# Kernel tuning notes

Hardware: AMD Instinct MI355X
Metric: run time of the kernel (lower is better)

Reference implementation:

```python
import jax, jax.numpy as jnp
import numpy as np

EPS = 1e-5          # denominator epsilon from module
PROJ_EPS = 4e-3     # geoopt float32 projection epsilon
MIN_NORM = 1e-15


def _sabs(x):
    return jnp.abs(x) + MIN_NORM


def _sign(x):
    # geoopt sign: sign(0) == 1
    return jnp.sign(jnp.sign(x) + 0.5)


def _clamp_abs(x, eps):
    return _sign(x) * jnp.maximum(jnp.abs(x), eps)


def _lambda_x(x, k):
    # conformal factor 2 / (1 + k ||x||^2)
    return 2.0 / jnp.maximum(1.0 + k * jnp.sum(x * x, axis=-1, keepdims=True), MIN_NORM)


def _parallel_transport0back(x, v, k):
    # transport v at x back to the origin: v / (1 + k ||x||^2)
    return v / jnp.maximum(1.0 + k * jnp.sum(x * x, axis=-1, keepdims=True), MIN_NORM)


def _artan_k(x, k):
    sk = jnp.sqrt(_sabs(k))
    hyp = jnp.arctanh(jnp.minimum(sk * x, 1.0 - 1e-7)) / sk   # k < 0
    sph = jnp.arctan(sk * x) / sk                              # k > 0
    return jnp.where(k < 0, hyp, sph)


def _tan_k(x, k):
    sk = jnp.sqrt(_sabs(k))
    return jnp.where(k < 0, jnp.tanh(sk * x) / sk, jnp.tan(sk * x) / sk)


def _project(x, k):
    maxnorm = (1.0 - PROJ_EPS) / jnp.sqrt(_sabs(k))
    maxnorm = jnp.where(k < 0, maxnorm, 1e15)
    norm = jnp.maximum(jnp.linalg.norm(x, axis=-1, keepdims=True), MIN_NORM)
    return jnp.where(norm > maxnorm, x / norm * maxnorm, x)


def _mobius_scalar_mul(r, x, k):
    xn = jnp.maximum(jnp.linalg.norm(x, axis=-1, keepdims=True), MIN_NORM)
    return _tan_k(r * _artan_k(xn, k), k) * (x / xn)


def setup_inputs() -> dict:
    key = jax.random.key(0)
    kQ, kK, kV = jax.random.split(key, 3)
    B, H, N, D = 4, 16, 4096, 64
    Q = jax.random.normal(kQ, (B, H, N, D), dtype=jnp.float32)
    K = jax.random.normal(kK, (B, H, N, D), dtype=jnp.float32)
    # V holds points on the Poincare ball: scale so ||V|| < 1
    V = 0.05 * jax.random.normal(kV, (B, H, N, D), dtype=jnp.float32)
    mask = jnp.ones((N,), dtype=jnp.float32)
    c = jnp.array([-1.0], dtype=jnp.float32)  # hyperbolic curvature (geoopt k-convention)
    return {"Q": Q, "K": K, "V": V, "mask": mask, "c": c}


def reference(Q, K, V, mask, c):
    H = Q.shape[-3]
    curv = jnp.broadcast_to(c.reshape(-1), (H,)) if c.shape[0] == 1 else c
    curv = curv[:, None, None]  # [H,1,1] broadcasts over [B,H,N,D]

    x = V
    v1 = _parallel_transport0back(x, Q, curv)
    v2 = _parallel_transport0back(x, K, curv)
    gamma = _lambda_x(x, curv)                     # [B,H,N,1]
    denom = _clamp_abs(gamma - 1.0, 1e-10)
    m = mask[None, :, None]                        # [1,N,1]
    x = gamma / denom * x * m
    v1 = jax.nn.elu(v1) + 1.0
    v2 = denom * (jax.nn.elu(v2) + 1.0) * m

    v2_sum = jnp.sum(v2, axis=-2)                  # [B,H,D]
    D = jnp.einsum('...nd,...d->...n', v1, v2_sum)
    D_inv = 1.0 / jnp.where(D == 0, EPS, D)
    context = jnp.einsum('...nd,...ne->...de', v2, x)   # [B,H,D,D]
    X = jnp.einsum('...de,...nd,...n->...ne', context, v1, D_inv)

    X = _project(X, curv)
    X = _mobius_scalar_mul(0.5, X, curv)
    X = _project(X, curv)
    return X
```

## Files before the change

kernel.cpp:

```cpp
#include <hip/hip_runtime.h>
#include <math.h>

#define EPS_C      1e-05f
#define PROJ_EPS_C 0.004f
#define MIN_NORM_C 1e-15f

#define NTOK   4096
#define DH     64
#define TILE   64
#define CHUNK2 128
#define NCHUNK2 (NTOK / CHUNK2)
#define PADROW 68
#define SUB    16

#define FMA4(ACC, S, B)                      \
    ACC.x = fmaf((S), (B).x, ACC.x);         \
    ACC.y = fmaf((S), (B).y, ACC.y);         \
    ACC.z = fmaf((S), (B).z, ACC.z);         \
    ACC.w = fmaf((S), (B).w, ACC.w);

#define ADD4(ACC, B)                         \
    ACC.x += (B).x; ACC.y += (B).y;          \
    ACC.z += (B).z; ACC.w += (B).w;

__device__ __forceinline__ float elup(float z) {
    return z > 0.f ? z + 1.f : __expf(z);
}

__global__ __launch_bounds__(256, 4) void glin_phase1(
    const float* __restrict__ Kk, const float* __restrict__ Vv,
    const float* __restrict__ mask, const float* __restrict__ cc,
    int csize, int H, int chunk_toks, int BH,
    float* __restrict__ pt_out,
    float* __restrict__ part_v2, float* __restrict__ part_ctx)
{
    __shared__ __align__(16) float stg[4][2][SUB][PADROW];
    __shared__ __align__(16) float v2red[4][DH];

    const int bh    = blockIdx.x;
    const int chunk = blockIdx.y;
    const int h     = bh % H;
    const float k   = cc[(csize == 1) ? 0 : h];

    const float* Kp = Kk + (size_t)bh * NTOK * DH;
    const float* Vp = Vv + (size_t)bh * NTOK * DH;
    float* ptp      = pt_out + (size_t)bh * NTOK;

    const int tid  = threadIdx.x;
    const int w    = tid >> 6;
    const int lane = tid & 63;
    const int r    = lane >> 3;
    const int cg   = lane & 7;
    const int srow = lane >> 4;
    const int c4   = lane & 15;

    float (*v2w)[PADROW] = stg[w][0];
    float (*xsw)[PADROW] = stg[w][1];

    float4 acc[8][2];
#pragma unroll
    for (int i = 0; i < 8; ++i) {
        acc[i][0] = make_float4(0.f, 0.f, 0.f, 0.f);
        acc[i][1] = make_float4(0.f, 0.f, 0.f, 0.f);
    }
    float4 va0 = make_float4(0.f, 0.f, 0.f, 0.f);
    float4 va1 = make_float4(0.f, 0.f, 0.f, 0.f);

    const int wtok  = chunk_toks >> 2;
    const int wbase = chunk * chunk_toks + w * wtok;

    for (int s = 0; s < wtok; s += SUB) {
        asm volatile("s_waitcnt lgkmcnt(0)" ::: "memory");
        __builtin_amdgcn_sched_barrier(0);
#pragma unroll
        for (int p = 0; p < 4; ++p) {
            const int row  = p * 4 + srow;
            const int gtok = wbase + s + row;
            float4 v4 = *(const float4*)(Vp + (size_t)gtok * DH + c4 * 4);
            float4 k4 = *(const float4*)(Kp + (size_t)gtok * DH + c4 * 4);
            float ss = v4.x * v4.x + v4.y * v4.y + v4.z * v4.z + v4.w * v4.w;
            ss += __shfl_xor(ss, 1);
            ss += __shfl_xor(ss, 2);
            ss += __shfl_xor(ss, 4);
            ss += __shfl_xor(ss, 8);
            float dpt   = fmaxf(1.f + k * ss, MIN_NORM_C);
            float pt    = 1.f / dpt;
            float gamma = 2.f * pt;
            float gm1   = gamma - 1.f;
            float sg    = (gm1 < 0.f) ? -1.f : 1.f;
            float denomG = sg * fmaxf(fabsf(gm1), 1e-10f);
            float m     = mask[gtok];
            float xsc   = gamma / denomG * m;
            float a2    = denomG * m;
            if (c4 == 0) ptp[gtok] = pt;
            v4.x *= xsc; v4.y *= xsc; v4.z *= xsc; v4.w *= xsc;
            k4.x = a2 * elup(k4.x * pt);
            k4.y = a2 * elup(k4.y * pt);
            k4.z = a2 * elup(k4.z * pt);
            k4.w = a2 * elup(k4.w * pt);
            *(float4*)&xsw[row][c4 * 4] = v4;
            *(float4*)&v2w[row][c4 * 4] = k4;
        }
        asm volatile("s_waitcnt lgkmcnt(0)" ::: "memory");
        __builtin_amdgcn_sched_barrier(0);
#pragma unroll 4
        for (int t = 0; t < SUB; ++t) {
            const float4 a0 = *(const float4*)&v2w[t][r * 8];
            const float4 a1 = *(const float4*)&v2w[t][r * 8 + 4];
            const float4 b0 = *(const float4*)&xsw[t][cg * 8];
            const float4 b1 = *(const float4*)&xsw[t][cg * 8 + 4];
            ADD4(va0, a0);
            ADD4(va1, a1);
            FMA4(acc[0][0], a0.x, b0); FMA4(acc[0][1], a0.x, b1);
            FMA4(acc[1][0], a0.y, b0); FMA4(acc[1][1], a0.y, b1);
            FMA4(acc[2][0], a0.z, b0); FMA4(acc[2][1], a0.z, b1);
            FMA4(acc[3][0], a0.w, b0); FMA4(acc[3][1], a0.w, b1);
            FMA4(acc[4][0], a1.x, b0); FMA4(acc[4][1], a1.x, b1);
            FMA4(acc[5][0], a1.y, b0); FMA4(acc[5][1], a1.y, b1);
            FMA4(acc[6][0], a1.z, b0); FMA4(acc[6][1], a1.z, b1);
            FMA4(acc[7][0], a1.w, b0); FMA4(acc[7][1], a1.w, b1);
        }
    }

    if (cg == 0) {
        *(float4*)&v2red[w][r * 8]     = va0;
        *(float4*)&v2red[w][r * 8 + 4] = va1;
    }
    __syncthreads();

    float* red   = &stg[0][0][0][0];
    const int eo = cg * 8;
    if (w == 1) {
#pragma unroll
        for (int i = 0; i < 8; ++i) {
            *(float4*)&red[(r * 8 + i) * DH + eo]     = acc[i][0];
            *(float4*)&red[(r * 8 + i) * DH + eo + 4] = acc[i][1];
        }
    } else if (w == 3) {
#pragma unroll
        for (int i = 0; i < 8; ++i) {
            *(float4*)&red[4096 + (r * 8 + i) * DH + eo]     = acc[i][0];
            *(float4*)&red[4096 + (r * 8 + i) * DH + eo + 4] = acc[i][1];
        }
    }
    __syncthreads();
    if (w == 0) {
#pragma unroll
        for (int i = 0; i < 8; ++i) {
            float4 t0 = *(const float4*)&red[(r * 8 + i) * DH + eo];
            float4 t1 = *(const float4*)&red[(r * 8 + i) * DH + eo + 4];
            ADD4(acc[i][0], t0);
            ADD4(acc[i][1], t1);
        }
    } else if (w == 2) {
#pragma unroll
        for (int i = 0; i < 8; ++i) {
            float4 t0 = *(const float4*)&red[4096 + (r * 8 + i) * DH + eo];
            float4 t1 = *(const float4*)&red[4096 + (r * 8 + i) * DH + eo + 4];
            ADD4(acc[i][0], t0);
            ADD4(acc[i][1], t1);
        }
    } else if (w == 1) {
        float sv = v2red[0][lane] + v2red[1][lane] + v2red[2][lane] + v2red[3][lane];
        part_v2[((size_t)chunk * BH + bh) * DH + lane] = sv;
    }
    __syncthreads();
    if (w == 2) {
#pragma unroll
        for (int i = 0; i < 8; ++i) {
            *(float4*)&red[(r * 8 + i) * DH + eo]     = acc[i][0];
            *(float4*)&red[(r * 8 + i) * DH + eo + 4] = acc[i][1];
        }
    }
    __syncthreads();
    if (w == 0) {
        float* pc = part_ctx + ((size_t)chunk * BH + bh) * (DH * DH);
#pragma unroll
        for (int i = 0; i < 8; ++i) {
            float4 t0 = *(const float4*)&red[(r * 8 + i) * DH + eo];
            float4 t1 = *(const float4*)&red[(r * 8 + i) * DH + eo + 4];
            ADD4(acc[i][0], t0);
            ADD4(acc[i][1], t1);
            *(float4*)&pc[(r * 8 + i) * DH + eo]     = acc[i][0];
            *(float4*)&pc[(r * 8 + i) * DH + eo + 4] = acc[i][1];
        }
    }
}

__global__ __launch_bounds__(256) void glin_reduce(
    const float* __restrict__ part_ctx, const float* __restrict__ part_v2,
    int P, int BH,
    float* __restrict__ ctx_out, float* __restrict__ v2sum_out)
{
    const int bh   = blockIdx.x;
    const int q    = blockIdx.y;
    const int tid  = threadIdx.x;
    const int base = q * 256 + tid;

    float s0 = 0.f;
    for (int c = 0; c < P; ++c)
        s0 += part_ctx[((size_t)c * BH + bh) * (DH * DH) + base];
    ctx_out[(size_t)bh * DH * DH + base] = s0;

    if (q == 0 && tid < DH) {
        float s = 0.f;
        for (int c = 0; c < P; ++c)
            s += part_v2[((size_t)c * BH + bh) * DH + tid];
        v2sum_out[(size_t)bh * DH + tid] = s;
    }
}

__device__ __forceinline__ void epilogue_store(
    float4 x, float dv, float k, float sk, float maxnorm,
    float* __restrict__ outp, int gtok, int tx)
{
    x.x *= dv; x.y *= dv; x.z *= dv; x.w *= dv;
    float n2 = x.x * x.x + x.y * x.y + x.z * x.z + x.w * x.w;
    n2 += __shfl_xor(n2, 1);
    n2 += __shfl_xor(n2, 2);
    n2 += __shfl_xor(n2, 4);
    n2 += __shfl_xor(n2, 8);
    float n  = fmaxf(sqrtf(n2), MIN_NORM_C);
    float scale = 1.f;
    float n1 = n;
    if (n > maxnorm) { scale = maxnorm / n; n1 = maxnorm; }
    float xn = fmaxf(n1, MIN_NORM_C);
    float s2;
    if (k < 0.f) {
        float t = fminf(sk * xn, 1.f - 1e-7f);
        s2 = 1.f / (1.f + sqrtf(fmaxf(1.f - t * t, 0.f)));
    } else {
        float t = sk * xn;
        s2 = 1.f / (1.f + sqrtf(1.f + t * t));
    }
    scale *= s2;
    float nrm2 = fmaxf(n1 * s2, MIN_NORM_C);
    if (nrm2 > maxnorm) scale *= maxnorm / nrm2;
    float4 o;
    o.x = x.x * scale; o.y = x.y * scale;
    o.z = x.z * scale; o.w = x.w * scale;
    *(float4*)(outp + (size_t)gtok * DH + tx * 4) = o;
}

__global__ __launch_bounds__(256, 4) void glin_phase2(
    const float* __restrict__ Qq, const float* __restrict__ cc,
    int csize, int H,
    const float* __restrict__ pt_in, const float* __restrict__ v2sum_in,
    const float* __restrict__ ctx_in, float* __restrict__ out)
{
    __shared__ __align__(16) float ctxs[DH][PADROW];
    __shared__ __align__(16) float v1s[TILE][PADROW];
    __shared__ __align__(16) float v2sum[DH];
    __shared__ float dinv[TILE];
    __shared__ __align__(16) float ptl[CHUNK2];

    const int bh    = blockIdx.x;
    const int chunk = blockIdx.y;
    const int h     = bh % H;
    const float k   = cc[(csize == 1) ? 0 : h];
    const float sk  = sqrtf(fabsf(k) + MIN_NORM_C);
    const float maxnorm = (k < 0.f) ? (1.f - PROJ_EPS_C) / sk : 1e15f;

    const int tid = threadIdx.x;
    const int ty  = tid >> 4;
    const int tx  = tid & 15;

    const float* Qp = Qq + (size_t)bh * NTOK * DH;
    float* outp     = out + (size_t)bh * NTOK * DH;

#pragma unroll
    for (int p = 0; p < 4; ++p) {
        int f = tid + p * 256;
        int d = f >> 4, c4 = f & 15;
        float4 v = *(const float4*)(ctx_in + (size_t)bh * DH * DH + d * DH + c4 * 4);
        *(float4*)&ctxs[d][c4 * 4] = v;
    }
    if (tid < 16) {
        float4 v = *(const float4*)(v2sum_in + (size_t)bh * DH + tid * 4);
        *(float4*)&v2sum[tid * 4] = v;
    }
    if (tid < CHUNK2 / 4) {
        float4 v = *(const float4*)(pt_in + (size_t)bh * NTOK + chunk * CHUNK2 + tid * 4);
        *(float4*)&ptl[tid * 4] = v;
    }
    __syncthreads();

    const int tbase = chunk * CHUNK2;
    for (int tt = 0; tt < CHUNK2; tt += TILE) {
#pragma unroll
        for (int p = 0; p < 4; ++p) {
            int f   = tid + p * 256;
            int row = f >> 4;
            int c4  = f & 15;
            int gtok = tbase + tt + row;
            float4 q4 = *(const float4*)(Qp + (size_t)gtok * DH + c4 * 4);
            float ptv = ptl[tt + row];
            float4 v1;
            v1.x = elup(q4.x * ptv);
            v1.y = elup(q4.y * ptv);
            v1.z = elup(q4.z * ptv);
            v1.w = elup(q4.w * ptv);
            float4 vs = *(const float4*)&v2sum[c4 * 4];
            float dp = v1.x * vs.x + v1.y * vs.y + v1.z * vs.z + v1.w * vs.w;
            dp += __shfl_xor(dp, 1);
            dp += __shfl_xor(dp, 2);
            dp += __shfl_xor(dp, 4);
            dp += __shfl_xor(dp, 8);
            if (c4 == 0) {
                float Dv = (dp == 0.f) ? EPS_C : dp;
                dinv[row] = 1.f / Dv;
            }
            *(float4*)&v1s[row][c4 * 4] = v1;
        }
        __syncthreads();
        float4 acc0 = {0.f, 0.f, 0.f, 0.f};
        float4 acc1 = {0.f, 0.f, 0.f, 0.f};
        float4 acc2 = {0.f, 0.f, 0.f, 0.f};
        float4 acc3 = {0.f, 0.f, 0.f, 0.f};
#pragma unroll 8
        for (int db = 0; db < DH / 4; ++db) {
            float4 b0 = *(const float4*)&ctxs[db * 4 + 0][tx * 4];
            float4 b1 = *(const float4*)&ctxs[db * 4 + 1][tx * 4];
            float4 b2 = *(const float4*)&ctxs[db * 4 + 2][tx * 4];
            float4 b3 = *(const float4*)&ctxs[db * 4 + 3][tx * 4];
            float4 a0 = *(const float4*)&v1s[ty * 4 + 0][db * 4];
            FMA4(acc0, a0.x, b0); FMA4(acc0, a0.y, b1);
            FMA4(acc0, a0.z, b2); FMA4(acc0, a0.w, b3);
            float4 a1 = *(const float4*)&v1s[ty * 4 + 1][db * 4];
            FMA4(acc1, a1.x, b0); FMA4(acc1, a1.y, b1);
            FMA4(acc1, a1.z, b2); FMA4(acc1, a1.w, b3);
            float4 a2 = *(const float4*)&v1s[ty * 4 + 2][db * 4];
            FMA4(acc2, a2.x, b0); FMA4(acc2, a2.y, b1);
            FMA4(acc2, a2.z, b2); FMA4(acc2, a2.w, b3);
            float4 a3 = *(const float4*)&v1s[ty * 4 + 3][db * 4];
            FMA4(acc3, a3.x, b0); FMA4(acc3, a3.y, b1);
            FMA4(acc3, a3.z, b2); FMA4(acc3, a3.w, b3);
        }
        epilogue_store(acc0, dinv[ty * 4 + 0], k, sk, maxnorm, outp, tbase + tt + ty * 4 + 0, tx);
        epilogue_store(acc1, dinv[ty * 4 + 1], k, sk, maxnorm, outp, tbase + tt + ty * 4 + 1, tx);
        epilogue_store(acc2, dinv[ty * 4 + 2], k, sk, maxnorm, outp, tbase + tt + ty * 4 + 2, tx);
        epilogue_store(acc3, dinv[ty * 4 + 3], k, sk, maxnorm, outp, tbase + tt + ty * 4 + 3, tx);
        __syncthreads();
    }
}

extern "C" void kernel_launch(void* const* d_in, const int* in_sizes, int n_in,
                              void* d_out, int out_size, void* d_ws, size_t ws_size,
                              hipStream_t stream)
{
    const float* Q    = (const float*)d_in[0];
    const float* K    = (const float*)d_in[1];
    const float* V    = (const float*)d_in[2];
    const float* mask = (const float*)d_in[3];
    const float* c    = (const float*)d_in[4];
    const int csize   = in_sizes[4];
    const int BH      = in_sizes[0] / (NTOK * DH);
    const int H       = 16;
    float* out        = (float*)d_out;

    int P = 16;
    while (P > 1) {
        size_t need = ((size_t)BH * NTOK
                     + (size_t)BH * DH
                     + (size_t)BH * DH * DH
                     + (size_t)P * BH * DH
                     + (size_t)P * BH * DH * DH)
                     * sizeof(float);
        if (need <= ws_size) break;
        P >>= 1;
    }
    const int chunk_toks = NTOK / P;

    float* pt       = (float*)d_ws;
    float* v2sum    = pt + (size_t)BH * NTOK;
    float* ctx      = v2sum + (size_t)BH * DH;
    float* part_v2  = ctx + (size_t)BH * DH * DH;
    float* part_ctx = part_v2 + (size_t)P * BH * DH;

    dim3 g1(BH, P);
    glin_phase1<<<g1, 256, 0, stream>>>(K, V, mask, c, csize, H, chunk_toks, BH,
                                        pt, part_v2, part_ctx);
    dim3 gr(BH, 16);
    glin_reduce<<<gr, 256, 0, stream>>>(part_ctx, part_v2, P, BH, ctx, v2sum);
    dim3 g2(BH, NCHUNK2);
    glin_phase2<<<g2, 256, 0, stream>>>(Q, c, csize, H, pt, v2sum, ctx, out);
}
```

Measured before the change: 275.3 us.

## Software-prefetch K/V and Q loads and make phase2 per-wave without block barriers

Phase1 now prefetches the next sub-tile of V, K and mask into registers while the current sub-tile is transformed and accumulated, overlapping global loads with compute. Phase2 is restructured so each wave independently processes 16-token sub-tiles with its own LDS buffers and double-buffered Q register prefetch, replacing block-wide __syncthreads with wave-local LDS fences, and the chunk size doubles to 256 tokens per block. Phase1 launch bounds drop to 3 waves per SIMD to make room for the prefetch registers, which lowers occupancy and launches half as many phase2 blocks.

```diff
diff --git a/kernel.cpp b/kernel.cpp
--- a/kernel.cpp
+++ b/kernel.cpp
@@ -7,8 +7,7 @@
 
 #define NTOK   4096
 #define DH     64
-#define TILE   64
-#define CHUNK2 128
+#define CHUNK2 256
 #define NCHUNK2 (NTOK / CHUNK2)
 #define PADROW 68
 #define SUB    16
@@ -23,11 +22,16 @@
     ACC.x += (B).x; ACC.y += (B).y;          \
     ACC.z += (B).z; ACC.w += (B).w;
 
+#define LDS_FENCE() do {                                   \
+    asm volatile("s_waitcnt lgkmcnt(0)" ::: "memory");     \
+    __builtin_amdgcn_sched_barrier(0);                     \
+} while (0)
+
 __device__ __forceinline__ float elup(float z) {
     return z > 0.f ? z + 1.f : __expf(z);
 }
 
-__global__ __launch_bounds__(256, 4) void glin_phase1(
+__global__ __launch_bounds__(256, 3) void glin_phase1(
     const float* __restrict__ Kk, const float* __restrict__ Vv,
     const float* __restrict__ mask, const float* __restrict__ cc,
     int csize, int H, int chunk_toks, int BH,
@@ -69,40 +73,50 @@
     const int wtok  = chunk_toks >> 2;
     const int wbase = chunk * chunk_toks + w * wtok;
 
+    float4 pv0, pv1, pv2, pv3, pk0, pk1, pk2, pk3;
+    float  pm0, pm1, pm2, pm3;
+
+#define P1_LOAD(S) { \
+    const float* vp_ = Vp + (size_t)(wbase + (S) + srow) * DH + c4 * 4; \
+    const float* kp_ = Kp + (size_t)(wbase + (S) + srow) * DH + c4 * 4; \
+    pv0 = *(const float4*)(vp_);            pk0 = *(const float4*)(kp_); \
+    pv1 = *(const float4*)(vp_ + 4 * DH);   pk1 = *(const float4*)(kp_ + 4 * DH); \
+    pv2 = *(const float4*)(vp_ + 8 * DH);   pk2 = *(const float4*)(kp_ + 8 * DH); \
+    pv3 = *(const float4*)(vp_ + 12 * DH);  pk3 = *(const float4*)(kp_ + 12 * DH); \
+    const float* mp_ = mask + wbase + (S) + srow; \
+    pm0 = mp_[0]; pm1 = mp_[4]; pm2 = mp_[8]; pm3 = mp_[12]; \
+}
+
+#define P1_XF(PV, PK, PM, P, S) { \
+    const int row_ = (P) * 4 + srow; \
+    float ss = PV.x*PV.x + PV.y*PV.y + PV.z*PV.z + PV.w*PV.w; \
+    ss += __shfl_xor(ss, 1); ss += __shfl_xor(ss, 2); \
+    ss += __shfl_xor(ss, 4); ss += __shfl_xor(ss, 8); \
+    const float dpt   = fmaxf(1.f + k * ss, MIN_NORM_C); \
+    const float pt_   = 1.f / dpt; \
+    const float gamma = 2.f * pt_; \
+    const float gm1   = gamma - 1.f; \
+    const float sg    = (gm1 < 0.f) ? -1.f : 1.f;    \
+    const float denomG = sg * fmaxf(fabsf(gm1), 1e-10f); \
+    const float xsc   = gamma / denomG * PM; \
+    const float a2    = denomG * PM; \
+    if (c4 == 0) ptp[wbase + (S) + row_] = pt_; \
+    float4 xv; xv.x = PV.x*xsc; xv.y = PV.y*xsc; xv.z = PV.z*xsc; xv.w = PV.w*xsc; \
+    float4 wv; wv.x = a2*elup(PK.x*pt_); wv.y = a2*elup(PK.y*pt_); \
+               wv.z = a2*elup(PK.z*pt_); wv.w = a2*elup(PK.w*pt_); \
+    *(float4*)&xsw[row_][c4 * 4] = xv; \
+    *(float4*)&v2w[row_][c4 * 4] = wv; \
+}
+
+    P1_LOAD(0);
     for (int s = 0; s < wtok; s += SUB) {
-        asm volatile("s_waitcnt lgkmcnt(0)" ::: "memory");
-        __builtin_amdgcn_sched_barrier(0);
-#pragma unroll
-        for (int p = 0; p < 4; ++p) {
-            const int row  = p * 4 + srow;
-            const int gtok = wbase + s + row;
-            float4 v4 = *(const float4*)(Vp + (size_t)gtok * DH + c4 * 4);
-            float4 k4 = *(const float4*)(Kp + (size_t)gtok * DH + c4 * 4);
-            float ss = v4.x * v4.x + v4.y * v4.y + v4.z * v4.z + v4.w * v4.w;
-            ss += __shfl_xor(ss, 1);
-            ss += __shfl_xor(ss, 2);
-            ss += __shfl_xor(ss, 4);
-            ss += __shfl_xor(ss, 8);
-            float dpt   = fmaxf(1.f + k * ss, MIN_NORM_C);
-            float pt    = 1.f / dpt;
-            float gamma = 2.f * pt;
-            float gm1   = gamma - 1.f;
-            float sg    = (gm1 < 0.f) ? -1.f : 1.f;
-            float denomG = sg * fmaxf(fabsf(gm1), 1e-10f);
-            float m     = mask[gtok];
-            float xsc   = gamma / denomG * m;
-            float a2    = denomG * m;
-            if (c4 == 0) ptp[gtok] = pt;
-            v4.x *= xsc; v4.y *= xsc; v4.z *= xsc; v4.w *= xsc;
-            k4.x = a2 * elup(k4.x * pt);
-            k4.y = a2 * elup(k4.y * pt);
-            k4.z = a2 * elup(k4.z * pt);
-            k4.w = a2 * elup(k4.w * pt);
-            *(float4*)&xsw[row][c4 * 4] = v4;
-            *(float4*)&v2w[row][c4 * 4] = k4;
-        }
-        asm volatile("s_waitcnt lgkmcnt(0)" ::: "memory");
-        __builtin_amdgcn_sched_barrier(0);
+        LDS_FENCE();
+        P1_XF(pv0, pk0, pm0, 0, s);
+        P1_XF(pv1, pk1, pm1, 1, s);
+        P1_XF(pv2, pk2, pm2, 2, s);
+        P1_XF(pv3, pk3, pm3, 3, s);
+        if (s + SUB < wtok) P1_LOAD(s + SUB);
+        LDS_FENCE();
 #pragma unroll 4
         for (int t = 0; t < SUB; ++t) {
             const float4 a0 = *(const float4*)&v2w[t][r * 8];
@@ -249,9 +263,9 @@
     const float* __restrict__ ctx_in, float* __restrict__ out)
 {
     __shared__ __align__(16) float ctxs[DH][PADROW];
-    __shared__ __align__(16) float v1s[TILE][PADROW];
+    __shared__ __align__(16) float v1b[4][SUB][PADROW];
     __shared__ __align__(16) float v2sum[DH];
-    __shared__ float dinv[TILE];
+    __shared__ __align__(16) float dinvw[4][SUB];
     __shared__ __align__(16) float ptl[CHUNK2];
 
     const int bh    = blockIdx.x;
@@ -261,9 +275,11 @@
     const float sk  = sqrtf(fabsf(k) + MIN_NORM_C);
     const float maxnorm = (k < 0.f) ? (1.f - PROJ_EPS_C) / sk : 1e15f;
 
-    const int tid = threadIdx.x;
-    const int ty  = tid >> 4;
-    const int tx  = tid & 15;
+    const int tid  = threadIdx.x;
+    const int w    = tid >> 6;
+    const int lane = tid & 63;
+    const int ty   = lane >> 4;
+    const int tx   = lane & 15;
 
     const float* Qp = Qq + (size_t)bh * NTOK * DH;
     float* outp     = out + (size_t)bh * NTOK * DH;
@@ -271,77 +287,84 @@
 #pragma unroll
     for (int p = 0; p < 4; ++p) {
         int f = tid + p * 256;
-        int d = f >> 4, c4 = f & 15;
-        float4 v = *(const float4*)(ctx_in + (size_t)bh * DH * DH + d * DH + c4 * 4);
-        *(float4*)&ctxs[d][c4 * 4] = v;
-    }
-    if (tid < 16) {
-        float4 v = *(const float4*)(v2sum_in + (size_t)bh * DH + tid * 4);
-        *(float4*)&v2sum[tid * 4] = v;
-    }
-    if (tid < CHUNK2 / 4) {
-        float4 v = *(const float4*)(pt_in + (size_t)bh * NTOK + chunk * CHUNK2 + tid * 4);
-        *(float4*)&ptl[tid * 4] = v;
-    }
+        int d = f >> 4, e4 = f & 15;
+        *(float4*)&ctxs[d][e4 * 4] =
+            *(const float4*)(ctx_in + (size_t)bh * DH * DH + d * DH + e4 * 4);
+    }
+    if (tid < 16)
+        *(float4*)&v2sum[tid * 4] =
+            *(const float4*)(v2sum_in + (size_t)bh * DH + tid * 4);
+    if (tid < CHUNK2 / 4)
+        *(float4*)&ptl[tid * 4] =
+            *(const float4*)(pt_in + (size_t)bh * NTOK + chunk * CHUNK2 + tid * 4);
     __syncthreads();
 
-    const int tbase = chunk * CHUNK2;
-    for (int tt = 0; tt < CHUNK2; tt += TILE) {
-#pragma unroll
-        for (int p = 0; p < 4; ++p) {
-            int f   = tid + p * 256;
-            int row = f >> 4;
-            int c4  = f & 15;
-            int gtok = tbase + tt + row;
-            float4 q4 = *(const float4*)(Qp + (size_t)gtok * DH + c4 * 4);
-            float ptv = ptl[tt + row];
-            float4 v1;
-            v1.x = elup(q4.x * ptv);
-            v1.y = elup(q4.y * ptv);
-            v1.z = elup(q4.z * ptv);
-            v1.w = elup(q4.w * ptv);
-            float4 vs = *(const float4*)&v2sum[c4 * 4];
-            float dp = v1.x * vs.x + v1.y * vs.y + v1.z * vs.z + v1.w * vs.w;
-            dp += __shfl_xor(dp, 1);
-            dp += __shfl_xor(dp, 2);
-            dp += __shfl_xor(dp, 4);
-            dp += __shfl_xor(dp, 8);
-            if (c4 == 0) {
-                float Dv = (dp == 0.f) ? EPS_C : dp;
-                dinv[row] = 1.f / Dv;
-            }
-            *(float4*)&v1s[row][c4 * 4] = v1;
-        }
-        __syncthreads();
-        float4 acc0 = {0.f, 0.f, 0.f, 0.f};
-        float4 acc1 = {0.f, 0.f, 0.f, 0.f};
-        float4 acc2 = {0.f, 0.f, 0.f, 0.f};
-        float4 acc3 = {0.f, 0.f, 0.f, 0.f};
-#pragma unroll 8
-        for (int db = 0; db < DH / 4; ++db) {
-            float4 b0 = *(const float4*)&ctxs[db * 4 + 0][tx * 4];
-            float4 b1 = *(const float4*)&ctxs[db * 4 + 1][tx * 4];
-            float4 b2 = *(const float4*)&ctxs[db * 4 + 2][tx * 4];
-            float4 b3 = *(const float4*)&ctxs[db * 4 + 3][tx * 4];
-            float4 a0 = *(const float4*)&v1s[ty * 4 + 0][db * 4];
-            FMA4(acc0, a0.x, b0); FMA4(acc0, a0.y, b1);
-            FMA4(acc0, a0.z, b2); FMA4(acc0, a0.w, b3);
-            float4 a1 = *(const float4*)&v1s[ty * 4 + 1][db * 4];
-            FMA4(acc1, a1.x, b0); FMA4(acc1, a1.y, b1);
-            FMA4(acc1, a1.z, b2); FMA4(acc1, a1.w, b3);
-            float4 a2 = *(const float4*)&v1s[ty * 4 + 2][db * 4];
-            FMA4(acc2, a2.x, b0); FMA4(acc2, a2.y, b1);
-            FMA4(acc2, a2.z, b2); FMA4(acc2, a2.w, b3);
-            float4 a3 = *(const float4*)&v1s[ty * 4 + 3][db * 4];
-            FMA4(acc3, a3.x, b0); FMA4(acc3, a3.y, b1);
-            FMA4(acc3, a3.z, b2); FMA4(acc3, a3.w, b3);
-        }
-        epilogue_store(acc0, dinv[ty * 4 + 0], k, sk, maxnorm, outp, tbase + tt + ty * 4 + 0, tx);
-        epilogue_store(acc1, dinv[ty * 4 + 1], k, sk, maxnorm, outp, tbase + tt + ty * 4 + 1, tx);
-        epilogue_store(acc2, dinv[ty * 4 + 2], k, sk, maxnorm, outp, tbase + tt + ty * 4 + 2, tx);
-        epilogue_store(acc3, dinv[ty * 4 + 3], k, sk, maxnorm, outp, tbase + tt + ty * 4 + 3, tx);
-        __syncthreads();
-    }
+    const int wloc = w * (CHUNK2 / 4);
+    const int wtb  = chunk * CHUNK2 + wloc;
+
+    float4 qa0, qa1, qa2, qa3, qb0, qb1, qb2, qb3;
+
+#define P2_LOADQ(R0, R1, R2, R3, S) { \
+    const float* qp_ = Qp + (size_t)(wtb + (S) + ty) * DH + tx * 4; \
+    R0 = *(const float4*)(qp_); \
+    R1 = *(const float4*)(qp_ + 4 * DH); \
+    R2 = *(const float4*)(qp_ + 8 * DH); \
+    R3 = *(const float4*)(qp_ + 12 * DH); \
+}
+
+#define P2_BUILD(R, P, S) { \
+    const int row_ = (P) * 4 + ty; \
+    const float ptv = ptl[wloc + (S) + row_]; \
+    float4 v1; \
+    v1.x = elup(R.x * ptv); v1.y = elup(R.y * ptv); \
+    v1.z = elup(R.z * ptv); v1.w = elup(R.w * ptv); \
+    const float4 vs = *(const float4*)&v2sum[tx * 4]; \
+    float dp = v1.x*vs.x + v1.y*vs.y + v1.z*vs.z + v1.w*vs.w; \
+    dp += __shfl_xor(dp, 1); dp += __shfl_xor(dp, 2); \
+    dp += __shfl_xor(dp, 4); dp += __shfl_xor(dp, 8); \
+    if (tx == 0) dinvw[w][row_] = 1.f / ((dp == 0.f) ? EPS_C : dp); \
+    *(float4*)&v1b[w][row_][tx * 4] = v1; \
+}
+
+#define P2_TILE(R0, R1, R2, R3, S) { \
+     \
+     \
+    LDS_FENCE(); \
+    P2_BUILD(R0, 0, S) P2_BUILD(R1, 1, S) P2_BUILD(R2, 2, S) P2_BUILD(R3, 3, S) \
+    LDS_FENCE(); \
+    float4 acc0 = make_float4(0.f, 0.f, 0.f, 0.f); \
+    float4 acc1 = make_float4(0.f, 0.f, 0.f, 0.f); \
+    float4 acc2 = make_float4(0.f, 0.f, 0.f, 0.f); \
+    float4 acc3 = make_float4(0.f, 0.f, 0.f, 0.f); \
+    _Pragma("unroll 8") \
+    for (int db = 0; db < DH / 4; ++db) { \
+        const float4 b0 = *(const float4*)&ctxs[db * 4 + 0][tx * 4]; \
+        const float4 b1 = *(const float4*)&ctxs[db * 4 + 1][tx * 4]; \
+        const float4 b2 = *(const float4*)&ctxs[db * 4 + 2][tx * 4]; \
+        const float4 b3 = *(const float4*)&ctxs[db * 4 + 3][tx * 4]; \
+        const float4 a0 = *(const float4*)&v1b[w][ty * 4 + 0][db * 4]; \
+        FMA4(acc0, a0.x, b0); FMA4(acc0, a0.y, b1); FMA4(acc0, a0.z, b2); FMA4(acc0, a0.w, b3); \
+        const float4 a1 = *(const float4*)&v1b[w][ty * 4 + 1][db * 4]; \
+        FMA4(acc1, a1.x, b0); FMA4(acc1, a1.y, b1); FMA4(acc1, a1.z, b2); FMA4(acc1, a1.w, b3); \
+        const float4 a2 = *(const float4*)&v1b[w][ty * 4 + 2][db * 4]; \
+        FMA4(acc2, a2.x, b0); FMA4(acc2, a2.y, b1); FMA4(acc2, a2.z, b2); FMA4(acc2, a2.w, b3); \
+        const float4 a3 = *(const float4*)&v1b[w][ty * 4 + 3][db * 4]; \
+        FMA4(acc3, a3.x, b0); FMA4(acc3, a3.y, b1); FMA4(acc3, a3.z, b2); FMA4(acc3, a3.w, b3); \
+    } \
+    epilogue_store(acc0, dinvw[w][ty * 4 + 0], k, sk, maxnorm, outp, wtb + (S) + ty * 4 + 0, tx); \
+    epilogue_store(acc1, dinvw[w][ty * 4 + 1], k, sk, maxnorm, outp, wtb + (S) + ty * 4 + 1, tx); \
+    epilogue_store(acc2, dinvw[w][ty * 4 + 2], k, sk, maxnorm, outp, wtb + (S) + ty * 4 + 2, tx); \
+    epilogue_store(acc3, dinvw[w][ty * 4 + 3], k, sk, maxnorm, outp, wtb + (S) + ty * 4 + 3, tx); \
+}
+
+    P2_LOADQ(qa0, qa1, qa2, qa3, 0);
+    P2_LOADQ(qb0, qb1, qb2, qb3, SUB);
+    P2_TILE (qa0, qa1, qa2, qa3, 0);
+    P2_LOADQ(qa0, qa1, qa2, qa3, 2 * SUB);
+    P2_TILE (qb0, qb1, qb2, qb3, SUB);
+    P2_LOADQ(qb0, qb1, qb2, qb3, 3 * SUB);
+    P2_TILE (qa0, qa1, qa2, qa3, 2 * SUB);
+    P2_TILE (qb0, qb1, qb2, qb3, 3 * SUB);
 }
 
 extern "C" void kernel_launch(void* const* d_in, const int* in_sizes, int n_in,
@@ -381,7 +404,7 @@
     glin_phase1<<<g1, 256, 0, stream>>>(K, V, mask, c, csize, H, chunk_toks, BH,
                                         pt, part_v2, part_ctx);
     dim3 gr(BH, 16);
-    glin_reduce<<<gr, 256, 0, stream>>>(part_ctx, part_v2, P, BH, ctx, v2sum);
+    glin_reduce<<<gr, 16 * sizeof(float) * 0 + 256, 0, stream>>>(part_ctx, part_v2, P, BH, ctx, v2sum);
     dim3 g2(BH, NCHUNK2);
     glin_phase2<<<g2, 256, 0, stream>>>(Q, c, csize, H, pt, v2sum, ctx, out);
 }
```

Result: faster. 268.2 us (-2.6%).
